# Kernel optimization log

Hardware: AMD Instinct MI355X
Metric: run time of the kernel (lower is better)

## Reference

```python
import jax, jax.numpy as jnp
import numpy as np

C = 64            # number of classes (all assumed present in y)
NUM_OVERLAP = 64  # int(args.d * args.overlap_ratio) = int(256 * 0.25)
ALPHA = 1.0       # args.alpha


def setup_inputs() -> dict:
    key = jax.random.key(0)
    k1, k2 = jax.random.split(key)
    x = jax.random.normal(k1, (65536, 512), dtype=jnp.float32)
    y = jax.random.randint(k2, (65536,), 0, C)
    return {"x": x, "y": y}


def reference(x, y):
    # one-hot class membership [C, N]
    member = (y[None, :] == jnp.arange(C)[:, None])
    counts = member.sum(axis=1).astype(x.dtype)                    # [C]
    # class centers: mean of member rows -> [C, D]
    centers = (member.astype(x.dtype) @ x) / counts[:, None]
    # pairwise L2 distance from every center to every sample, [C, N],
    # via ||c||^2 + ||x||^2 - 2 c.x (avoids [C, N, D] intermediate)
    c2 = jnp.sum(centers * centers, axis=1)[:, None]               # [C, 1]
    x2 = jnp.sum(x * x, axis=1)[None, :]                           # [1, N]
    d2 = c2 + x2 - 2.0 * (centers @ x.T)                           # [C, N]
    dist = jnp.sqrt(jnp.maximum(d2, 1e-12))
    neg_inf = jnp.asarray(-jnp.inf, dist.dtype)
    # positives: largest NUM_OVERLAP distances among same-class samples
    pos_vals = jax.lax.top_k(jnp.where(member, dist, neg_inf), NUM_OVERLAP)[0]
    pos_mean = pos_vals.mean(axis=1)                               # [C]
    # negatives: smallest NUM_OVERLAP distances among other-class samples
    neg_vals = -jax.lax.top_k(jnp.where(member, neg_inf, -dist), NUM_OVERLAP)[0]
    neg_mean = neg_vals.mean(axis=1)                               # [C]
    per_class = jnp.maximum(ALPHA + pos_mean - neg_mean, 0.0)
    loss = jnp.sum(per_class) / (C * NUM_OVERLAP)
    return loss.reshape(1)
```

## Files before the change

kernel.cpp:

```cpp
#include <hip/hip_runtime.h>
#include <math.h>

#define N_SAMP 65536
#define DIM    512
#define NCLS   64
#define KSEL   64
#define SNBIN  4096

#define OFF_COUNTS   0u
#define OFF_CSUM     256u
#define OFF_CENTERS  131328u
#define OFF_C2       196864u
#define OFF_MEANS    197120u
#define OFF_DONE     197632u
#define OFF_XB       262144u
#define OFF_DIST     67371008u
#define WS_NEED      84148224u
#define OFF_DIST_FB  262144u

typedef __attribute__((ext_vector_type(8))) short bf16x8;
typedef __attribute__((ext_vector_type(4))) float f32x4;

__device__ __forceinline__ unsigned short f2bf_rne(float f) {
  const unsigned u = __float_as_uint(f);
  return (unsigned short)((u + 0x7FFFu + ((u >> 16) & 1u)) >> 16);
}

__global__ __launch_bounds__(256) void k_init(int* __restrict__ counts,
                                              float* __restrict__ csum,
                                              unsigned* __restrict__ done) {
  const int i = blockIdx.x * 256 + threadIdx.x;
  const int stride = gridDim.x * 256;
  if (i < NCLS) counts[i] = 0;
  if (i == 0) *done = 0u;
  for (int j = i; j < NCLS * DIM; j += stride) csum[j] = 0.f;
}

__global__ __launch_bounds__(256) void k_class_sums(const float* __restrict__ x,
                                                    const int* __restrict__ y,
                                                    float* __restrict__ csum,
                                                    int* __restrict__ counts,
                                                    unsigned* __restrict__ xb32) {
  __shared__ int list[4096];
  __shared__ int lcnt;
  const int c  = blockIdx.x >> 4;
  const int r0 = (blockIdx.x & 15) * 4096;
  const int tid = threadIdx.x;
  if (tid == 0) lcnt = 0;
  __syncthreads();
  for (int i = tid; i < 4096; i += 256) {
    if (y[r0 + i] == c) { int p = atomicAdd(&lcnt, 1); list[p] = r0 + i; }
  }
  __syncthreads();
  const int n = lcnt;
  const int dbase = (tid >> 6) * 128 + (tid & 63) * 2;
  const int xoff = dbase >> 1;
  float a0 = 0.f, a1 = 0.f, b0 = 0.f, b1 = 0.f;
  int i = 0;
  for (; i + 2 <= n; i += 2) {
    const int r0i = list[i], r1i = list[i + 1];
    const float* p0 = x + (size_t)r0i * DIM + dbase;
    const float* p1 = x + (size_t)r1i * DIM + dbase;
    const float v00 = p0[0], v01 = p0[1], v10 = p1[0], v11 = p1[1];
    a0 += v00; a1 += v01;
    b0 += v10; b1 += v11;
    if (xb32) {
      xb32[(size_t)r0i * 256 + xoff] = (unsigned)f2bf_rne(v00) | ((unsigned)f2bf_rne(v01) << 16);
      xb32[(size_t)r1i * 256 + xoff] = (unsigned)f2bf_rne(v10) | ((unsigned)f2bf_rne(v11) << 16);
    }
  }
  if (i < n) {
    const int ri = list[i];
    const float* p0 = x + (size_t)ri * DIM + dbase;
    const float v00 = p0[0], v01 = p0[1];
    a0 += v00; a1 += v01;
    if (xb32) xb32[(size_t)ri * 256 + xoff] = (unsigned)f2bf_rne(v00) | ((unsigned)f2bf_rne(v01) << 16);
  }
  a0 += b0; a1 += b1;
  atomicAdd(&csum[c * DIM + dbase], a0);
  atomicAdd(&csum[c * DIM + dbase + 1], a1);
  if (tid == 0) atomicAdd(&counts[c], n);
}

__global__ __launch_bounds__(64) void k_centers(const float* __restrict__ csum,
                                                const int* __restrict__ counts,
                                                unsigned short* __restrict__ cenb,
                                                float* __restrict__ c2) {
  const int c = blockIdx.x, l = threadIdx.x;
  const float inv = 1.0f / (float)counts[c];
  float ss = 0.f;
  #pragma unroll
  for (int j = 0; j < 8; ++j) {
    int d = j * 64 + l;
    float v = csum[c * DIM + d] * inv;
    cenb[c * DIM + d] = f2bf_rne(v);
    ss += v * v;
  }
  #pragma unroll
  for (int o = 32; o; o >>= 1) ss += __shfl_down(ss, o, 64);
  if (l == 0) c2[c] = ss;
}

#define CSTR 520
__global__ __launch_bounds__(512, 4) void k_dist_bf(const unsigned short* __restrict__ xb,
                                                    const unsigned short* __restrict__ cenb,
                                                    const float* __restrict__ c2,
                                                    float* __restrict__ dist) {
  __shared__ unsigned short cenS[NCLS * CSTR];
  __shared__ float c2s[NCLS];

  const int tid = threadIdx.x;
  const int wave = tid >> 6;
  const int lane = tid & 63;
  const int s0 = blockIdx.x * 128 + wave * 16;
  const int samp = s0 + (lane & 15);
  const int kg = lane >> 4;

  for (int q = tid; q < 4096; q += 512) {
    const int row = q >> 6, cc = q & 63;
    const uint4 v = *reinterpret_cast<const uint4*>(cenb + row * DIM + cc * 8);
    *reinterpret_cast<uint4*>(&cenS[row * CSTR + cc * 8]) = v;
  }
  if (tid < NCLS) c2s[tid] = c2[tid];
  __syncthreads();

  f32x4 acc[4] = {f32x4{0,0,0,0}, f32x4{0,0,0,0}, f32x4{0,0,0,0}, f32x4{0,0,0,0}};
  float x2 = 0.f;
  const unsigned short* __restrict__ xrow = xb + (size_t)samp * DIM + kg * 8;
  const int arow = lane & 15;

  #pragma unroll 4
  for (int s = 0; s < 16; ++s) {
    const int k0 = s * 32;
    const bf16x8 bfrag = *reinterpret_cast<const bf16x8*>(xrow + k0);
    const uint4 bu = *reinterpret_cast<const uint4*>(&bfrag);
    {
      const unsigned dw[4] = {bu.x, bu.y, bu.z, bu.w};
      #pragma unroll
      for (int q = 0; q < 4; ++q) {
        const float flo = __uint_as_float(dw[q] << 16);
        const float fhi = __uint_as_float(dw[q] & 0xFFFF0000u);
        x2 = fmaf(flo, flo, x2);
        x2 = fmaf(fhi, fhi, x2);
      }
    }
    const int kidx = k0 + kg * 8;
    const bf16x8 a0 = *reinterpret_cast<const bf16x8*>(&cenS[(arow +  0) * CSTR + kidx]);
    const bf16x8 a1 = *reinterpret_cast<const bf16x8*>(&cenS[(arow + 16) * CSTR + kidx]);
    const bf16x8 a2 = *reinterpret_cast<const bf16x8*>(&cenS[(arow + 32) * CSTR + kidx]);
    const bf16x8 a3 = *reinterpret_cast<const bf16x8*>(&cenS[(arow + 48) * CSTR + kidx]);
    acc[0] = __builtin_amdgcn_mfma_f32_16x16x32_bf16(a0, bfrag, acc[0], 0, 0, 0);
    acc[1] = __builtin_amdgcn_mfma_f32_16x16x32_bf16(a1, bfrag, acc[1], 0, 0, 0);
    acc[2] = __builtin_amdgcn_mfma_f32_16x16x32_bf16(a2, bfrag, acc[2], 0, 0, 0);
    acc[3] = __builtin_amdgcn_mfma_f32_16x16x32_bf16(a3, bfrag, acc[3], 0, 0, 0);
  }

  x2 += __shfl_xor(x2, 16, 64);
  x2 += __shfl_xor(x2, 32, 64);

  const int col = s0 + (lane & 15);
  #pragma unroll
  for (int t = 0; t < 4; ++t) {
    #pragma unroll
    for (int r = 0; r < 4; ++r) {
      const int cls = t * 16 + (lane >> 4) * 4 + r;
      const float d2 = c2s[cls] + x2 - 2.0f * acc[t][r];
      dist[(size_t)cls * N_SAMP + col] = sqrtf(fmaxf(d2, 1e-12f));
    }
  }
}

__global__ __launch_bounds__(512, 4) void k_dist_f32(const float* __restrict__ x,
                                                     const unsigned short* __restrict__ cenb,
                                                     const float* __restrict__ c2,
                                                     float* __restrict__ dist) {
  __shared__ unsigned short cenS[NCLS * CSTR];
  __shared__ float c2s[NCLS];
  const int tid = threadIdx.x;
  const int wave = tid >> 6;
  const int lane = tid & 63;
  const int s0 = blockIdx.x * 128 + wave * 16;
  const int samp = s0 + (lane & 15);
  const int kg = lane >> 4;
  for (int q = tid; q < 4096; q += 512) {
    const int row = q >> 6, cc = q & 63;
    const uint4 v = *reinterpret_cast<const uint4*>(cenb + row * DIM + cc * 8);
    *reinterpret_cast<uint4*>(&cenS[row * CSTR + cc * 8]) = v;
  }
  if (tid < NCLS) c2s[tid] = c2[tid];
  __syncthreads();
  f32x4 acc[4] = {f32x4{0,0,0,0}, f32x4{0,0,0,0}, f32x4{0,0,0,0}, f32x4{0,0,0,0}};
  float x2 = 0.f;
  const float* __restrict__ xrow = x + (size_t)samp * DIM + kg * 8;
  const int arow = lane & 15;
  #pragma unroll 4
  for (int s = 0; s < 16; ++s) {
    const int k0 = s * 32;
    float xf[8];
    *reinterpret_cast<float4*>(&xf[0]) = *reinterpret_cast<const float4*>(xrow + k0);
    *reinterpret_cast<float4*>(&xf[4]) = *reinterpret_cast<const float4*>(xrow + k0 + 4);
    bf16x8 bfrag;
    #pragma unroll
    for (int j = 0; j < 8; ++j) {
      x2 = fmaf(xf[j], xf[j], x2);
      const unsigned u = __float_as_uint(xf[j]);
      bfrag[j] = (short)((u + 0x7FFFu + ((u >> 16) & 1u)) >> 16);
    }
    const int kidx = k0 + kg * 8;
    const bf16x8 a0 = *reinterpret_cast<const bf16x8*>(&cenS[(arow +  0) * CSTR + kidx]);
    const bf16x8 a1 = *reinterpret_cast<const bf16x8*>(&cenS[(arow + 16) * CSTR + kidx]);
    const bf16x8 a2 = *reinterpret_cast<const bf16x8*>(&cenS[(arow + 32) * CSTR + kidx]);
    const bf16x8 a3 = *reinterpret_cast<const bf16x8*>(&cenS[(arow + 48) * CSTR + kidx]);
    acc[0] = __builtin_amdgcn_mfma_f32_16x16x32_bf16(a0, bfrag, acc[0], 0, 0, 0);
    acc[1] = __builtin_amdgcn_mfma_f32_16x16x32_bf16(a1, bfrag, acc[1], 0, 0, 0);
    acc[2] = __builtin_amdgcn_mfma_f32_16x16x32_bf16(a2, bfrag, acc[2], 0, 0, 0);
    acc[3] = __builtin_amdgcn_mfma_f32_16x16x32_bf16(a3, bfrag, acc[3], 0, 0, 0);
  }
  x2 += __shfl_xor(x2, 16, 64);
  x2 += __shfl_xor(x2, 32, 64);
  const int col = s0 + (lane & 15);
  #pragma unroll
  for (int t = 0; t < 4; ++t) {
    #pragma unroll
    for (int r = 0; r < 4; ++r) {
      const int cls = t * 16 + (lane >> 4) * 4 + r;
      const float d2 = c2s[cls] + x2 - 2.0f * acc[t][r];
      dist[(size_t)cls * N_SAMP + col] = sqrtf(fmaxf(d2, 1e-12f));
    }
  }
}

__device__ __forceinline__ void redB(float v0, float v2, float v3, float* redf, float* bcast) {
  #pragma unroll
  for (int o = 32; o; o >>= 1) {
    v0 += __shfl_xor(v0, o, 64);
    v2 = fminf(v2, __shfl_xor(v2, o, 64));
    v3 = fmaxf(v3, __shfl_xor(v3, o, 64));
  }
  const int wid = threadIdx.x >> 6;
  if ((threadIdx.x & 63) == 0) { redf[wid] = v0; redf[16 + wid] = v2; redf[32 + wid] = v3; }
  __syncthreads();
  if (threadIdx.x < 16) {
    const int l = threadIdx.x;
    float a0 = redf[l], a2 = redf[16 + l], a3 = redf[32 + l];
    #pragma unroll
    for (int o = 8; o; o >>= 1) {
      a0 += __shfl_xor(a0, o, 64);
      a2 = fminf(a2, __shfl_xor(a2, o, 64));
      a3 = fmaxf(a3, __shfl_xor(a3, o, 64));
    }
    if (l == 0) { bcast[0] = a0; bcast[2] = a2; bcast[3] = a3; }
  }
  __syncthreads();
}

__device__ __forceinline__ int binS(float w, float lo, float sc) {
  int b = (int)((w - lo) * sc);
  b = b < SNBIN - 1 ? b : SNBIN - 1;
  return b > 0 ? b : 0;
}

__device__ __forceinline__ float wavePeel(const float* buf, int cnt, int need, int lane) {
  float thr = -1e30f, s = 0.f;
  int taken = 0;
  for (int g = 0; g < 64 && taken < need; ++g) {
    float m = 1e30f;
    for (int t = 0; t < 16; ++t) {
      const int idx = lane + t * 64;
      if (idx < cnt) { const float u = buf[idx]; if (u > thr) m = fminf(m, u); }
    }
    #pragma unroll
    for (int o = 32; o; o >>= 1) m = fminf(m, __shfl_xor(m, o, 64));
    int ce = 0;
    for (int t = 0; t < 16; ++t) {
      const int idx = lane + t * 64;
      if (idx < cnt && buf[idx] == m) ++ce;
    }
    #pragma unroll
    for (int o = 32; o; o >>= 1) ce += __shfl_xor(ce, o, 64);
    const int take = (need - taken) < ce ? (need - taken) : ce;
    s += (float)take * m;
    taken += take;
    thr = m;
  }
  return s;
}

__global__ __launch_bounds__(1024, 2) void k_select4(const float* __restrict__ dist,
                                                     const int* __restrict__ y,
                                                     float* __restrict__ means,
                                                     unsigned* __restrict__ done,
                                                     float* __restrict__ out) {
  __shared__ unsigned bitmap[2048];
  __shared__ unsigned hist[SNBIN];
  __shared__ unsigned wscan[16];
  __shared__ float redf[48];
  __shared__ float bcast[4];
  __shared__ float bbuf[1024];
  __shared__ int bcnt_s, bsel_s;
  __shared__ unsigned strict_s;
  __shared__ float bsum_s;
  __shared__ int lastflag;

  const int tid = threadIdx.x;
  const int lane = tid & 63;
  const int wid = tid >> 6;
  const int c = blockIdx.x >> 1;
  const int role = blockIdx.x & 1;
  const float* __restrict__ row = dist + (size_t)c * N_SAMP;

  if (tid == 0) { bcnt_s = 0; bsel_s = 0; strict_s = 0u; bsum_s = 0.f; lastflag = 0; }

  {
    const int4* __restrict__ y4 = (const int4*)(y + tid * 64);
    unsigned w0 = 0u, w1 = 0u;
    #pragma unroll
    for (int i = 0; i < 8; ++i) {
      const int4 a = y4[i];
      w0 |= (unsigned)(a.x == c) << (i * 4);
      w0 |= (unsigned)(a.y == c) << (i * 4 + 1);
      w0 |= (unsigned)(a.z == c) << (i * 4 + 2);
      w0 |= (unsigned)(a.w == c) << (i * 4 + 3);
    }
    #pragma unroll
    for (int i = 0; i < 8; ++i) {
      const int4 a = y4[8 + i];
      w1 |= (unsigned)(a.x == c) << (i * 4);
      w1 |= (unsigned)(a.y == c) << (i * 4 + 1);
      w1 |= (unsigned)(a.z == c) << (i * 4 + 2);
      w1 |= (unsigned)(a.w == c) << (i * 4 + 3);
    }
    bitmap[tid * 2] = w0;
    bitmap[tid * 2 + 1] = w1;
  }
  __syncthreads();

  float mn = 1e30f, mx = -1e30f;
  #pragma unroll 4
  for (int i = 0; i < 16; ++i) {
    const int base = i * 4096 + tid * 4;
    const float4 v4 = *reinterpret_cast<const float4*>(row + base);
    const unsigned bits = bitmap[base >> 5] >> (base & 31);
    const float vv[4] = {v4.x, v4.y, v4.z, v4.w};
    #pragma unroll
    for (int j = 0; j < 4; ++j) {
      if ((int)((bits >> j) & 1u) != role) {
        const float w = role ? vv[j] : -vv[j];
        mn = fminf(mn, w);
        mx = fmaxf(mx, w);
      }
    }
  }
  redB(0.f, mn, mx, redf, bcast);
  const float lo = bcast[2], hi = bcast[3];
  const bool deg = !(hi > lo);
  float meanval;

  if (deg) {
    meanval = role ? lo : -lo;
  } else {
    const float sc = (float)SNBIN / (hi - lo);
    for (int i = tid; i < SNBIN; i += 1024) hist[i] = 0u;
    __syncthreads();

    #pragma unroll 4
    for (int i = 0; i < 16; ++i) {
      const int base = i * 4096 + tid * 4;
      const float4 v4 = *reinterpret_cast<const float4*>(row + base);
      const unsigned bits = bitmap[base >> 5] >> (base & 31);
      const float vv[4] = {v4.x, v4.y, v4.z, v4.w};
      #pragma unroll
      for (int j = 0; j < 4; ++j) {
        if ((int)((bits >> j) & 1u) != role) {
          const float w = role ? vv[j] : -vv[j];
          atomicAdd(&hist[binS(w, lo, sc)], 1u);
        }
      }
    }
    __syncthreads();

    {
      unsigned b4[4]; unsigned s4 = 0;
      #pragma unroll
      for (int j = 0; j < 4; ++j) { b4[j] = hist[tid * 4 + j]; s4 += b4[j]; }
      unsigned cum = s4;
      #pragma unroll
      for (int d = 1; d < 64; d <<= 1) {
        const unsigned t = (unsigned)__shfl_up((int)cum, d, 64);
        if (lane >= d) cum += t;
      }
      if (lane == 63) wscan[wid] = cum;
      __syncthreads();
      if (tid < 16) {
        unsigned v = wscan[tid];
        #pragma unroll
        for (int d = 1; d < 16; d <<= 1) {
          const unsigned t = (unsigned)__shfl_up((int)v, d, 64);
          if (tid >= d) v += t;
        }
        wscan[tid] = v;
      }
      __syncthreads();
      const unsigned gcum = cum + (wid ? wscan[wid - 1] : 0u);
      const unsigned gprev = gcum - s4;
      if (gcum >= (unsigned)KSEL && gprev < (unsigned)KSEL) {
        unsigned run = gprev;
        #pragma unroll
        for (int j = 0; j < 4; ++j) {
          if (run + b4[j] >= (unsigned)KSEL) { bsel_s = tid * 4 + j; strict_s = run; break; }
          run += b4[j];
        }
      }
      __syncthreads();
    }
    const int B = bsel_s;
    const int need = KSEL - (int)strict_s;

    float ss = 0.f;
    #pragma unroll 4
    for (int i = 0; i < 16; ++i) {
      const int base = i * 4096 + tid * 4;
      const float4 v4 = *reinterpret_cast<const float4*>(row + base);
      const unsigned bits = bitmap[base >> 5] >> (base & 31);
      const float vv[4] = {v4.x, v4.y, v4.z, v4.w};
      #pragma unroll
      for (int j = 0; j < 4; ++j) {
        if ((int)((bits >> j) & 1u) != role) {
          const float w = role ? vv[j] : -vv[j];
          const int b = binS(w, lo, sc);
          if (b < B) ss += w;
          else if (b == B) { const int p = atomicAdd(&bcnt_s, 1); if (p < 1024) bbuf[p] = w; }
        }
      }
    }
    redB(ss, 0.f, 0.f, redf, bcast);
    const float SS = bcast[0];
    const int cnt = bcnt_s;

    if (cnt <= 1024) {
      if (wid == 0) {
        const float s = wavePeel(bbuf, cnt, need, lane);
        if (lane == 0) bsum_s = s;
      }
      __syncthreads();
    } else {
      float thr = -1e30f, accum = 0.f;
      int taken = 0;
      for (int g = 0; g < 64 && taken < need; ++g) {
        float m = 1e30f;
        for (int i = 0; i < 16; ++i) {
          const int base = i * 4096 + tid * 4;
          const float4 v4 = *reinterpret_cast<const float4*>(row + base);
          const unsigned bits = bitmap[base >> 5] >> (base & 31);
          const float vv[4] = {v4.x, v4.y, v4.z, v4.w};
          for (int j = 0; j < 4; ++j) {
            if ((int)((bits >> j) & 1u) != role) {
              const float w = role ? vv[j] : -vv[j];
              if (binS(w, lo, sc) == B && w > thr) m = fminf(m, w);
            }
          }
        }
        redB(0.f, m, 0.f, redf, bcast);
        const float M = bcast[2];
        float ce = 0.f;
        for (int i = 0; i < 16; ++i) {
          const int base = i * 4096 + tid * 4;
          const float4 v4 = *reinterpret_cast<const float4*>(row + base);
          const unsigned bits = bitmap[base >> 5] >> (base & 31);
          const float vv[4] = {v4.x, v4.y, v4.z, v4.w};
          for (int j = 0; j < 4; ++j) {
            if ((int)((bits >> j) & 1u) != role) {
              const float w = role ? vv[j] : -vv[j];
              if (w == M) ce += 1.f;
            }
          }
        }
        redB(ce, 0.f, 0.f, redf, bcast);
        const int CE = (int)bcast[0];
        const int take = (need - taken) < CE ? (need - taken) : CE;
        accum += (float)take * M;
        taken += take;
        thr = M;
      }
      if (tid == 0) bsum_s = accum;
      __syncthreads();
    }

    const float total = SS + bsum_s;
    meanval = role ? total * (1.0f / 64.0f) : -total * (1.0f / 64.0f);
  }

  if (tid == 0) {
    __hip_atomic_store(&means[role * 64 + c], meanval, __ATOMIC_RELAXED, __HIP_MEMORY_SCOPE_AGENT);
    const unsigned old = __hip_atomic_fetch_add(done, 1u, __ATOMIC_ACQ_REL, __HIP_MEMORY_SCOPE_AGENT);
    lastflag = (old == 127u) ? 1 : 0;
  }
  __syncthreads();
  if (lastflag && tid < 64) {
    const float pm = __hip_atomic_load(&means[tid], __ATOMIC_ACQUIRE, __HIP_MEMORY_SCOPE_AGENT);
    const float nm = __hip_atomic_load(&means[64 + tid], __ATOMIC_ACQUIRE, __HIP_MEMORY_SCOPE_AGENT);
    float pc = fmaxf(1.0f + pm - nm, 0.0f);
    #pragma unroll
    for (int o = 32; o; o >>= 1) pc += __shfl_down(pc, o, 64);
    if (tid == 0) out[0] = pc * (1.0f / 4096.0f);
  }
}

extern "C" void kernel_launch(void* const* d_in, const int* in_sizes, int n_in,
                              void* d_out, int out_size, void* d_ws, size_t ws_size,
                              hipStream_t stream) {
  const float* x = (const float*)d_in[0];
  const int* y = (const int*)d_in[1];
  float* out = (float*)d_out;
  char* w = (char*)d_ws;
  int* counts          = (int*)(w + OFF_COUNTS);
  float* csum          = (float*)(w + OFF_CSUM);
  unsigned short* cenb = (unsigned short*)(w + OFF_CENTERS);
  float* c2            = (float*)(w + OFF_C2);
  float* means         = (float*)(w + OFF_MEANS);
  unsigned* done       = (unsigned*)(w + OFF_DONE);

  const bool big = (ws_size >= (size_t)WS_NEED);
  float* dist = (float*)(w + (big ? OFF_DIST : OFF_DIST_FB));
  unsigned* xb32 = big ? (unsigned*)(w + OFF_XB) : (unsigned*)nullptr;

  hipLaunchKernelGGL(k_init, dim3(64), dim3(256), 0, stream, counts, csum, done);
  hipLaunchKernelGGL(k_class_sums, dim3(1024), dim3(256), 0, stream, x, y, csum, counts, xb32);
  hipLaunchKernelGGL(k_centers, dim3(64), dim3(64), 0, stream, csum, counts, cenb, c2);
  if (big) {
    hipLaunchKernelGGL(k_dist_bf, dim3(N_SAMP / 128), dim3(512), 0, stream,
                       (const unsigned short*)xb32, cenb, c2, dist);
  } else {
    hipLaunchKernelGGL(k_dist_f32, dim3(N_SAMP / 128), dim3(512), 0, stream, x, cenb, c2, dist);
  }
  hipLaunchKernelGGL(k_select4, dim3(128), dim3(1024), 0, stream, dist, y, means, done, out);
}
```

Before: 104.0 us.

## Drop bf16 copy of x and read centers directly from global in distance kernel

The class-sum kernel no longer writes a bf16 copy of x. The distance kernel now always reads fp32 x and converts it to bf16 in registers. The distance kernel also stops staging centers and c2 in shared memory and loads MFMA fragments straight from global memory, which should hit in L2/L1 because the centers total only 64 KB. This removes a 64 MB write plus its re-read and the shared-memory staging with its barrier, but the kernel now reads 128 MB of fp32 x instead of 64 MB of bf16 and puts the center loads on the global path.

```diff
diff --git a/kernel.cpp b/kernel.cpp
--- a/kernel.cpp
+++ b/kernel.cpp
@@ -13,10 +13,7 @@
 #define OFF_C2       196864u
 #define OFF_MEANS    197120u
 #define OFF_DONE     197632u
-#define OFF_XB       262144u
-#define OFF_DIST     67371008u
-#define WS_NEED      84148224u
-#define OFF_DIST_FB  262144u
+#define OFF_DIST     262144u
 
 typedef __attribute__((ext_vector_type(8))) short bf16x8;
 typedef __attribute__((ext_vector_type(4))) float f32x4;
@@ -39,8 +36,7 @@
 __global__ __launch_bounds__(256) void k_class_sums(const float* __restrict__ x,
                                                     const int* __restrict__ y,
                                                     float* __restrict__ csum,
-                                                    int* __restrict__ counts,
-                                                    unsigned* __restrict__ xb32) {
+                                                    int* __restrict__ counts) {
   __shared__ int list[4096];
   __shared__ int lcnt;
   const int c  = blockIdx.x >> 4;
@@ -54,28 +50,15 @@
   __syncthreads();
   const int n = lcnt;
   const int dbase = (tid >> 6) * 128 + (tid & 63) * 2;
-  const int xoff = dbase >> 1;
   float a0 = 0.f, a1 = 0.f, b0 = 0.f, b1 = 0.f;
   int i = 0;
   for (; i + 2 <= n; i += 2) {
-    const int r0i = list[i], r1i = list[i + 1];
-    const float* p0 = x + (size_t)r0i * DIM + dbase;
-    const float* p1 = x + (size_t)r1i * DIM + dbase;
-    const float v00 = p0[0], v01 = p0[1], v10 = p1[0], v11 = p1[1];
-    a0 += v00; a1 += v01;
-    b0 += v10; b1 += v11;
-    if (xb32) {
-      xb32[(size_t)r0i * 256 + xoff] = (unsigned)f2bf_rne(v00) | ((unsigned)f2bf_rne(v01) << 16);
-      xb32[(size_t)r1i * 256 + xoff] = (unsigned)f2bf_rne(v10) | ((unsigned)f2bf_rne(v11) << 16);
-    }
-  }
-  if (i < n) {
-    const int ri = list[i];
-    const float* p0 = x + (size_t)ri * DIM + dbase;
-    const float v00 = p0[0], v01 = p0[1];
-    a0 += v00; a1 += v01;
-    if (xb32) xb32[(size_t)ri * 256 + xoff] = (unsigned)f2bf_rne(v00) | ((unsigned)f2bf_rne(v01) << 16);
-  }
+    const float* p0 = x + (size_t)list[i] * DIM + dbase;
+    const float* p1 = x + (size_t)list[i + 1] * DIM + dbase;
+    a0 += p0[0]; a1 += p0[1];
+    b0 += p1[0]; b1 += p1[1];
+  }
+  if (i < n) { const float* p0 = x + (size_t)list[i] * DIM + dbase; a0 += p0[0]; a1 += p0[1]; }
   a0 += b0; a1 += b1;
   atomicAdd(&csum[c * DIM + dbase], a0);
   atomicAdd(&csum[c * DIM + dbase + 1], a1);
@@ -101,104 +84,33 @@
   if (l == 0) c2[c] = ss;
 }
 
-#define CSTR 520
-__global__ __launch_bounds__(512, 4) void k_dist_bf(const unsigned short* __restrict__ xb,
-                                                    const unsigned short* __restrict__ cenb,
-                                                    const float* __restrict__ c2,
-                                                    float* __restrict__ dist) {
-  __shared__ unsigned short cenS[NCLS * CSTR];
-  __shared__ float c2s[NCLS];
-
+__global__ __launch_bounds__(512, 4) void k_dist_g(const float* __restrict__ x,
+                                                   const unsigned short* __restrict__ cenb,
+                                                   const float* __restrict__ c2,
+                                                   float* __restrict__ dist) {
   const int tid = threadIdx.x;
   const int wave = tid >> 6;
   const int lane = tid & 63;
   const int s0 = blockIdx.x * 128 + wave * 16;
   const int samp = s0 + (lane & 15);
   const int kg = lane >> 4;
-
-  for (int q = tid; q < 4096; q += 512) {
-    const int row = q >> 6, cc = q & 63;
-    const uint4 v = *reinterpret_cast<const uint4*>(cenb + row * DIM + cc * 8);
-    *reinterpret_cast<uint4*>(&cenS[row * CSTR + cc * 8]) = v;
-  }
-  if (tid < NCLS) c2s[tid] = c2[tid];
-  __syncthreads();
-
-  f32x4 acc[4] = {f32x4{0,0,0,0}, f32x4{0,0,0,0}, f32x4{0,0,0,0}, f32x4{0,0,0,0}};
-  float x2 = 0.f;
-  const unsigned short* __restrict__ xrow = xb + (size_t)samp * DIM + kg * 8;
   const int arow = lane & 15;
 
-  #pragma unroll 4
-  for (int s = 0; s < 16; ++s) {
-    const int k0 = s * 32;
-    const bf16x8 bfrag = *reinterpret_cast<const bf16x8*>(xrow + k0);
-    const uint4 bu = *reinterpret_cast<const uint4*>(&bfrag);
-    {
-      const unsigned dw[4] = {bu.x, bu.y, bu.z, bu.w};
-      #pragma unroll
-      for (int q = 0; q < 4; ++q) {
-        const float flo = __uint_as_float(dw[q] << 16);
-        const float fhi = __uint_as_float(dw[q] & 0xFFFF0000u);
-        x2 = fmaf(flo, flo, x2);
-        x2 = fmaf(fhi, fhi, x2);
-      }
-    }
-    const int kidx = k0 + kg * 8;
-    const bf16x8 a0 = *reinterpret_cast<const bf16x8*>(&cenS[(arow +  0) * CSTR + kidx]);
-    const bf16x8 a1 = *reinterpret_cast<const bf16x8*>(&cenS[(arow + 16) * CSTR + kidx]);
-    const bf16x8 a2 = *reinterpret_cast<const bf16x8*>(&cenS[(arow + 32) * CSTR + kidx]);
-    const bf16x8 a3 = *reinterpret_cast<const bf16x8*>(&cenS[(arow + 48) * CSTR + kidx]);
-    acc[0] = __builtin_amdgcn_mfma_f32_16x16x32_bf16(a0, bfrag, acc[0], 0, 0, 0);
-    acc[1] = __builtin_amdgcn_mfma_f32_16x16x32_bf16(a1, bfrag, acc[1], 0, 0, 0);
-    acc[2] = __builtin_amdgcn_mfma_f32_16x16x32_bf16(a2, bfrag, acc[2], 0, 0, 0);
-    acc[3] = __builtin_amdgcn_mfma_f32_16x16x32_bf16(a3, bfrag, acc[3], 0, 0, 0);
-  }
-
-  x2 += __shfl_xor(x2, 16, 64);
-  x2 += __shfl_xor(x2, 32, 64);
-
-  const int col = s0 + (lane & 15);
-  #pragma unroll
-  for (int t = 0; t < 4; ++t) {
-    #pragma unroll
-    for (int r = 0; r < 4; ++r) {
-      const int cls = t * 16 + (lane >> 4) * 4 + r;
-      const float d2 = c2s[cls] + x2 - 2.0f * acc[t][r];
-      dist[(size_t)cls * N_SAMP + col] = sqrtf(fmaxf(d2, 1e-12f));
-    }
-  }
-}
-
-__global__ __launch_bounds__(512, 4) void k_dist_f32(const float* __restrict__ x,
-                                                     const unsigned short* __restrict__ cenb,
-                                                     const float* __restrict__ c2,
-                                                     float* __restrict__ dist) {
-  __shared__ unsigned short cenS[NCLS * CSTR];
-  __shared__ float c2s[NCLS];
-  const int tid = threadIdx.x;
-  const int wave = tid >> 6;
-  const int lane = tid & 63;
-  const int s0 = blockIdx.x * 128 + wave * 16;
-  const int samp = s0 + (lane & 15);
-  const int kg = lane >> 4;
-  for (int q = tid; q < 4096; q += 512) {
-    const int row = q >> 6, cc = q & 63;
-    const uint4 v = *reinterpret_cast<const uint4*>(cenb + row * DIM + cc * 8);
-    *reinterpret_cast<uint4*>(&cenS[row * CSTR + cc * 8]) = v;
-  }
-  if (tid < NCLS) c2s[tid] = c2[tid];
-  __syncthreads();
   f32x4 acc[4] = {f32x4{0,0,0,0}, f32x4{0,0,0,0}, f32x4{0,0,0,0}, f32x4{0,0,0,0}};
   float x2 = 0.f;
   const float* __restrict__ xrow = x + (size_t)samp * DIM + kg * 8;
-  const int arow = lane & 15;
+  const unsigned short* __restrict__ crow = cenb + (size_t)arow * DIM + kg * 8;
+
   #pragma unroll 4
   for (int s = 0; s < 16; ++s) {
     const int k0 = s * 32;
     float xf[8];
     *reinterpret_cast<float4*>(&xf[0]) = *reinterpret_cast<const float4*>(xrow + k0);
     *reinterpret_cast<float4*>(&xf[4]) = *reinterpret_cast<const float4*>(xrow + k0 + 4);
+    const bf16x8 a0 = *reinterpret_cast<const bf16x8*>(crow + k0);
+    const bf16x8 a1 = *reinterpret_cast<const bf16x8*>(crow + 16 * DIM + k0);
+    const bf16x8 a2 = *reinterpret_cast<const bf16x8*>(crow + 32 * DIM + k0);
+    const bf16x8 a3 = *reinterpret_cast<const bf16x8*>(crow + 48 * DIM + k0);
     bf16x8 bfrag;
     #pragma unroll
     for (int j = 0; j < 8; ++j) {
@@ -206,25 +118,22 @@
       const unsigned u = __float_as_uint(xf[j]);
       bfrag[j] = (short)((u + 0x7FFFu + ((u >> 16) & 1u)) >> 16);
     }
-    const int kidx = k0 + kg * 8;
-    const bf16x8 a0 = *reinterpret_cast<const bf16x8*>(&cenS[(arow +  0) * CSTR + kidx]);
-    const bf16x8 a1 = *reinterpret_cast<const bf16x8*>(&cenS[(arow + 16) * CSTR + kidx]);
-    const bf16x8 a2 = *reinterpret_cast<const bf16x8*>(&cenS[(arow + 32) * CSTR + kidx]);
-    const bf16x8 a3 = *reinterpret_cast<const bf16x8*>(&cenS[(arow + 48) * CSTR + kidx]);
     acc[0] = __builtin_amdgcn_mfma_f32_16x16x32_bf16(a0, bfrag, acc[0], 0, 0, 0);
     acc[1] = __builtin_amdgcn_mfma_f32_16x16x32_bf16(a1, bfrag, acc[1], 0, 0, 0);
     acc[2] = __builtin_amdgcn_mfma_f32_16x16x32_bf16(a2, bfrag, acc[2], 0, 0, 0);
     acc[3] = __builtin_amdgcn_mfma_f32_16x16x32_bf16(a3, bfrag, acc[3], 0, 0, 0);
   }
+
   x2 += __shfl_xor(x2, 16, 64);
   x2 += __shfl_xor(x2, 32, 64);
+
   const int col = s0 + (lane & 15);
   #pragma unroll
   for (int t = 0; t < 4; ++t) {
     #pragma unroll
     for (int r = 0; r < 4; ++r) {
       const int cls = t * 16 + (lane >> 4) * 4 + r;
-      const float d2 = c2s[cls] + x2 - 2.0f * acc[t][r];
+      const float d2 = c2[cls] + x2 - 2.0f * acc[t][r];
       dist[(size_t)cls * N_SAMP + col] = sqrtf(fmaxf(d2, 1e-12f));
     }
   }
@@ -519,19 +428,11 @@
   float* c2            = (float*)(w + OFF_C2);
   float* means         = (float*)(w + OFF_MEANS);
   unsigned* done       = (unsigned*)(w + OFF_DONE);
-
-  const bool big = (ws_size >= (size_t)WS_NEED);
-  float* dist = (float*)(w + (big ? OFF_DIST : OFF_DIST_FB));
-  unsigned* xb32 = big ? (unsigned*)(w + OFF_XB) : (unsigned*)nullptr;
+  float* dist          = (float*)(w + OFF_DIST);
 
   hipLaunchKernelGGL(k_init, dim3(64), dim3(256), 0, stream, counts, csum, done);
-  hipLaunchKernelGGL(k_class_sums, dim3(1024), dim3(256), 0, stream, x, y, csum, counts, xb32);
+  hipLaunchKernelGGL(k_class_sums, dim3(1024), dim3(256), 0, stream, x, y, csum, counts);
   hipLaunchKernelGGL(k_centers, dim3(64), dim3(64), 0, stream, csum, counts, cenb, c2);
-  if (big) {
-    hipLaunchKernelGGL(k_dist_bf, dim3(N_SAMP / 128), dim3(512), 0, stream,
-                       (const unsigned short*)xb32, cenb, c2, dist);
-  } else {
-    hipLaunchKernelGGL(k_dist_f32, dim3(N_SAMP / 128), dim3(512), 0, stream, x, cenb, c2, dist);
-  }
+  hipLaunchKernelGGL(k_dist_g, dim3(N_SAMP / 128), dim3(512), 0, stream, x, cenb, c2, dist);
   hipLaunchKernelGGL(k_select4, dim3(128), dim3(1024), 0, stream, dist, y, means, done, out);
 }
```

Result: slower. 124.2 us (+19.3%).
